# Optimization experiments

Hardware: AMD Instinct MI355X
Metric: run time of the kernel (lower is better)

## Reference

```python
import jax, jax.numpy as jnp
import numpy as np

B, N, F, H, E = 64, 64, 2, 1024, 65536
T_IN, T_OUT = 10, 6  # SAMPLING_INPUT_FRAMES, SAMPLING_OUTPUT_FRAMES
NT = B * N
THRESH, EXIST = 10.0, 0.04
MLP_DIMS = [(2048, H), (4096, 2048), (2048, 4096), (1024, 2048), (512, 1024), (F * N, 512)]


def setup_inputs():
    key = jax.random.key(0)
    ks = jax.random.split(key, 32)
    inp = {
        'feature_input': jax.random.normal(ks[0], (T_IN, NT, F), jnp.float32),
        'edge_indices_input': jax.random.randint(ks[1], (T_IN, 2, E), 0, NT),
        'edge_indices_output': jax.random.randint(ks[2], (T_OUT, 2, E), 0, NT),
        'number_of_trajectories': B,
        'stats': jax.random.uniform(ks[3], (2, F), jnp.float32, 0.5, 1.5),  # (std, mean)
        'w_gcn': jax.random.normal(ks[4], (F, F), jnp.float32) / np.sqrt(F),
        'b_gcn': jnp.zeros((F,), jnp.float32),
        'w_ih': jax.random.normal(ks[5], (4 * H, F * N), jnp.float32) / np.sqrt(F * N),
        'w_hh': jax.random.normal(ks[6], (4 * H, H), jnp.float32) / np.sqrt(H),
        'b_ih': jnp.zeros((4 * H,), jnp.float32),
        'b_hh': jnp.zeros((4 * H,), jnp.float32),
    }
    for i, (o, d) in enumerate(MLP_DIMS):
        inp[f'w{i+1}'] = jax.random.normal(ks[7 + i], (o, d), jnp.float32) / np.sqrt(d)
        inp[f'b{i+1}'] = jnp.zeros((o,), jnp.float32)
    return inp


def _gcn_edges(x, ei, W, b):
    # PyG GCNConv: out = D^{-1/2} (A + I) D^{-1/2} (x W^T) + b, edge list form
    xw = x @ W.T
    src, dst = ei[0], ei[1]
    n = x.shape[0]
    deg = 1.0 + jax.ops.segment_sum(jnp.ones_like(src, jnp.float32), dst, num_segments=n)
    dinv = jax.lax.rsqrt(deg)
    out = jax.ops.segment_sum(xw[src] * (dinv[src] * dinv[dst])[:, None], dst, num_segments=n)
    return out + xw * (dinv * dinv)[:, None] + b


def _gcn_dense(x, A, W, b):
    # x [B,N,F]; A [B,N,N] already contains self loops (find_edge_index output)
    deg = A.sum(-1)
    dinv = jnp.where(deg > 0, jax.lax.rsqrt(deg), 0.0)
    An = A * dinv[:, :, None] * dinv[:, None, :]
    return jnp.einsum('bij,bjf->bif', An, x @ W.T) + b


def _build_adj(pred, stats, bsz):
    # faithful to find_edge_index: denormalize, cdist<=10, existence mask, self-loops kept
    f = (pred * stats[0] + stats[1]).reshape(bsz, N, F)
    d2 = jnp.sum((f[:, :, None, :] - f[:, None, :, :]) ** 2, -1)
    mask = (jnp.sqrt(jnp.maximum(d2, 0.0)) <= THRESH).astype(jnp.float32)
    exist = ((f[..., 0] > EXIST) & (f[..., 1] > EXIST)).astype(jnp.float32)
    A = mask * exist[:, :, None] * exist[:, None, :]
    # gcn_norm's add_remaining_self_loops -> every node ends with a self loop
    return jnp.maximum(A, jnp.eye(N, dtype=A.dtype))


def _forward(feature_input, edge_indices_input, bsz, stats, w_gcn, b_gcn, w_ih, w_hh, b_ih, b_hh, mlp_params):
    h = jnp.zeros((bsz, H), feature_input.dtype)
    c = jnp.zeros((bsz, H), feature_input.dtype)

    def lstm(x, h, c):  # torch LSTM gate order i, f, g, o
        g = x @ w_ih.T + b_ih + h @ w_hh.T + b_hh
        i, f, gg, o = jnp.split(g, 4, axis=-1)
        c = jax.nn.sigmoid(f) * c + jax.nn.sigmoid(i) * jnp.tanh(gg)
        h = jax.nn.sigmoid(o) * jnp.tanh(c)
        return h, c

    def mlp(x):
        for w, b_ in mlp_params[:-1]:
            x = jax.nn.relu(x @ w.T + b_)
        w, b_ = mlp_params[-1]
        return x @ w.T + b_

    x_enc = [feature_input[0]]
    for i in range(T_IN - 1):  # torch loop breaks before last frame
        g = _gcn_edges(feature_input[i], edge_indices_input[i], w_gcn, b_gcn)
        h, c = lstm(g.reshape(bsz, F * N), h, c)
        x_enc.append(mlp(h).reshape(bsz * N, F))

    cur_x = feature_input[T_IN - 1]
    cur_ei = edge_indices_input[T_IN - 1]
    A = None
    y_dec = []
    for i in range(T_OUT):
        if i == 0:
            g = _gcn_edges(cur_x, cur_ei, w_gcn, b_gcn)
        else:
            g = _gcn_dense(cur_x.reshape(bsz, N, F), A, w_gcn, b_gcn).reshape(bsz * N, F)
        h, c = lstm(g.reshape(bsz, F * N), h, c)
        pred = mlp(h).reshape(bsz * N, F)
        y_dec.append(pred)
        cur_x = pred
        A = _build_adj(pred, stats, bsz)
    # [T_IN + T_OUT, B*N, F]: x_pred_encode stacked then y_pred_decode stacked
    return jnp.concatenate([jnp.stack(x_enc), jnp.stack(y_dec)], 0)


def reference(feature_input, edge_indices_input, edge_indices_output, number_of_trajectories, stats, w_gcn, b_gcn, w_ih, w_hh, b_ih, b_hh, w1, b1, w2, b2, w3, b3, w4, b4, w5, b5, w6, b6):
    mlp_params = [(w1, b1), (w2, b2), (w3, b3), (w4, b4), (w5, b5), (w6, b6)]
    return _forward(feature_input, edge_indices_input, number_of_trajectories, stats, w_gcn, b_gcn, w_ih, w_hh, b_ih, b_hh, mlp_params)
```

## Files before the change

kernel.cpp:

```cpp
#include <hip/hip_runtime.h>
#include <hip/hip_bf16.h>
#include <math.h>

#define NTOT 4096
#define NEDGE 65536
#define BSZ 64
#define NN 64
#define HDIM 1024
#define TIN 10
#define TOUT 6
#define FRAME_ELEMS (NTOT * 2)

typedef short s16x8 __attribute__((ext_vector_type(8)));
typedef float f32x4 __attribute__((ext_vector_type(4)));

__device__ __forceinline__ unsigned short f2bf(float f) {
    union { float f; unsigned u; } x; x.f = f;
    unsigned r = x.u + 0x7fffu + ((x.u >> 16) & 1u);
    return (unsigned short)(r >> 16);
}

struct TT { const float* W; float* WT; int NO; int K; int toff; };
struct TT8 { TT t[8]; };

__global__ __launch_bounds__(256) void transpose_all(TT8 tasks) {
    int bid = blockIdx.x;
    int ti = 0;
    #pragma unroll
    for (int j = 1; j < 8; ++j) if (bid >= tasks.t[j].toff) ti = j;
    TT tk = tasks.t[ti];
    int local = bid - tk.toff;
    int tilesK = tk.K >> 5;
    int kb = local % tilesK, nb = local / tilesK;
    int k0 = kb * 32, n0 = nb * 32;
    __shared__ float t[32][33];
    int tx = threadIdx.x & 31, ty = threadIdx.x >> 5;
    #pragma unroll
    for (int i = 0; i < 4; ++i)
        t[ty + i * 8][tx] = tk.W[(size_t)(n0 + ty + i * 8) * tk.K + k0 + tx];
    __syncthreads();
    #pragma unroll
    for (int i = 0; i < 4; ++i)
        tk.WT[(size_t)(k0 + ty + i * 8) * tk.NO + n0 + tx] = t[tx][ty + i * 8];
}


__global__ void bgcn_init_xw(const float* __restrict__ feat, const float* __restrict__ wg,
                             float* __restrict__ deg, float* __restrict__ xw) {
    int i = blockIdx.x * blockDim.x + threadIdx.x;
    if (i >= 10 * NTOT) return;
    deg[i] = 1.0f;
    float x0 = feat[i * 2], x1 = feat[i * 2 + 1];
    xw[i * 2]     = x0 * wg[0] + x1 * wg[1];
    xw[i * 2 + 1] = x0 * wg[2] + x1 * wg[3];
}

__global__ void bgcn_count(const int* __restrict__ ei, float* __restrict__ deg) {
    int e = blockIdx.x * blockDim.x + threadIdx.x;
    if (e >= 10 * NEDGE) return;
    int t = e >> 16, el = e & 65535;
    int dst = ei[t * 2 * NEDGE + NEDGE + el];
    atomicAdd(&deg[t * NTOT + dst], 1.0f);
}

__global__ void bgcn_node(const float* __restrict__ bg, float* __restrict__ deg,
                          const float* __restrict__ xw, float* __restrict__ gT_all) {
    int i = blockIdx.x * blockDim.x + threadIdx.x;
    if (i >= 10 * NTOT) return;
    float dinv = rsqrtf(deg[i]);
    deg[i] = dinv;
    int t = i >> 12, node = i & 4095;
    int b = node >> 6, nn = node & 63;
    float w2 = dinv * dinv;
    gT_all[t * 8192 + (nn * 2 + 0) * 64 + b] = xw[i * 2]     * w2 + bg[0];
    gT_all[t * 8192 + (nn * 2 + 1) * 64 + b] = xw[i * 2 + 1] * w2 + bg[1];
}

__global__ __launch_bounds__(256) void bgcn_scatter_lds(const int* __restrict__ ei,
                                                        const float* __restrict__ dinv,
                                                        const float* __restrict__ xw,
                                                        float* __restrict__ gT_all) {
    __shared__ float sg[8192];
    int t = blockIdx.x >> 3;
    int chunk = blockIdx.x & 7;
    for (int i = threadIdx.x; i < 8192; i += 256) sg[i] = 0.f;
    __syncthreads();
    const int* eis = ei + t * 2 * NEDGE;
    int e0 = chunk * 8192;
    for (int e = e0 + threadIdx.x; e < e0 + 8192; e += 256) {
        int s = eis[e];
        int d = eis[NEDGE + e];
        float w = dinv[t * NTOT + s] * dinv[t * NTOT + d];
        int b = d >> 6, nn = d & 63;
        atomicAdd(&sg[(nn * 2 + 0) * 64 + b], xw[(t * NTOT + s) * 2]     * w);
        atomicAdd(&sg[(nn * 2 + 1) * 64 + b], xw[(t * NTOT + s) * 2 + 1] * w);
    }
    __syncthreads();
    float* gt = gT_all + t * 8192;
    for (int i = threadIdx.x; i < 8192; i += 256) {
        float v = sg[i];
        if (v != 0.f) atomicAdd(&gt[i], v);
    }
}

template<int KC>
__global__ __launch_bounds__(256) void gemm_bx7(
    const float* __restrict__ inT, const float* __restrict__ inT2,
    const float* __restrict__ WT,  const float* __restrict__ WT2,
    float* __restrict__ P, int NO, int SK1)
{
    constexpr int STG = (KC > 64) ? 64 : KC;
    __shared__ float xs[STG * 64];
    int tid = threadIdx.x;
    int ks = blockIdx.y;
    const float* xsrc; const float* wsrc;
    if (ks < SK1) { xsrc = inT  + (size_t)ks * KC * 64;         wsrc = WT  + (size_t)ks * KC * NO; }
    else          { xsrc = inT2 + (size_t)(ks - SK1) * KC * 64; wsrc = WT2 + (size_t)(ks - SK1) * KC * NO; }
    int ns = tid >> 3, q = tid & 7;
    int n = blockIdx.x * 32 + ns;
    const float* xq = xs + q * 8;
    float acc[8];
    #pragma unroll
    for (int j = 0; j < 8; ++j) acc[j] = 0.f;

    for (int kb = 0; kb < KC; kb += STG) {
        if (kb) __syncthreads();
        #pragma unroll
        for (int i = 0; i < STG / 16; ++i)
            ((float4*)xs)[tid + i * 256] = ((const float4*)(xsrc + (size_t)kb * 64))[tid + i * 256];
        __syncthreads();
        const float* wp = wsrc + (size_t)kb * NO + n;
        float wbuf[4];
        #pragma unroll
        for (int kk = 0; kk < 4; ++kk) wbuf[kk] = wp[(size_t)kk * NO];
        for (int k = 0; k < STG; k += 4) {
            float wn[4] = {0.f, 0.f, 0.f, 0.f};
            if (k + 4 < STG) {
                #pragma unroll
                for (int kk = 0; kk < 4; ++kk) wn[kk] = wp[(size_t)(k + 4 + kk) * NO];
            }
            #pragma unroll
            for (int kk = 0; kk < 4; ++kk) {
                const float* xrow = xq + (k + kk) * 64;
                float w = wbuf[kk];
                float4 x0 = *(const float4*)(xrow + 0);
                float4 x1 = *(const float4*)(xrow + 4);
                acc[0] = fmaf(w, x0.x, acc[0]);  acc[1] = fmaf(w, x0.y, acc[1]);
                acc[2] = fmaf(w, x0.z, acc[2]);  acc[3] = fmaf(w, x0.w, acc[3]);
                acc[4] = fmaf(w, x1.x, acc[4]);  acc[5] = fmaf(w, x1.y, acc[5]);
                acc[6] = fmaf(w, x1.z, acc[6]);  acc[7] = fmaf(w, x1.w, acc[7]);
            }
            #pragma unroll
            for (int kk = 0; kk < 4; ++kk) wbuf[kk] = wn[kk];
        }
    }
    float* pp = P + ((size_t)ks * NO + n) * 64 + q * 8;
    *(float4*)(pp + 0) = make_float4(acc[0], acc[1], acc[2], acc[3]);
    *(float4*)(pp + 4) = make_float4(acc[4], acc[5], acc[6], acc[7]);
}

__global__ void reduce_relu_kernel(const float* __restrict__ P,
                                   const float* __restrict__ bias,
                                   float* __restrict__ aT,
                                   int NO, int SK, int relu) {
    int idx = blockIdx.x * blockDim.x + threadIdx.x;
    if (idx >= NO * 64) return;
    int n = idx >> 6;
    float v = bias[n];
    for (int ks = 0; ks < SK; ++ks) v += P[(size_t)ks * NO * 64 + idx];
    if (relu) v = fmaxf(v, 0.f);
    aT[idx] = v;
}

__global__ void lstm_update2(const float* __restrict__ P,
                             const float* __restrict__ b_ih, const float* __restrict__ b_hh,
                             float* __restrict__ hT, float* __restrict__ cT,
                             unsigned short* __restrict__ stash, int mbase) {
    int t = blockIdx.x * blockDim.x + threadIdx.x;
    if (t >= HDIM * BSZ) return;
    int j = t >> 6, b = t & 63;
    float g4[4];
    #pragma unroll
    for (int gi = 0; gi < 4; ++gi) {
        int row = gi * HDIM + j;
        float v = b_ih[row] + b_hh[row];
        size_t base = (size_t)row * 64 + b;
        #pragma unroll
        for (int ks = 0; ks < 9; ++ks) v += P[(size_t)ks * 4096 * 64 + base];
        g4[gi] = v;
    }
    float si = 1.f / (1.f + expf(-g4[0]));
    float sf = 1.f / (1.f + expf(-g4[1]));
    float gg = tanhf(g4[2]);
    float so = 1.f / (1.f + expf(-g4[3]));
    float cn = sf * cT[t] + si * gg;
    cT[t] = cn;
    float h = so * tanhf(cn);
    hT[t] = h;
    if (stash) stash[(size_t)(mbase + b) * HDIM + j] = f2bf(h);
}

__global__ void finalize3(const float* __restrict__ P, const float* __restrict__ b5,
                          const float* __restrict__ wt5, const float* __restrict__ b6,
                          const float* __restrict__ stats, const float* __restrict__ wg,
                          const float* __restrict__ bg,
                          float* __restrict__ frame, float* __restrict__ gT, int dec)
{
    int b = blockIdx.x;
    int n = threadIdx.x;
    __shared__ float a5[512];
    __shared__ float p[128];
    __shared__ float f0[NN], f1[NN], sxw0[NN], sxw1[NN], sdinv[NN];
    __shared__ int ex[NN];
    #pragma unroll
    for (int j = 0; j < 4; ++j) {
        int k = n * 4 + j;
        float v = b5[k];
        #pragma unroll 4
        for (int ks = 0; ks < 16; ++ks) v += P[((size_t)ks * 512 + k) * 64 + b];
        a5[k] = fmaxf(v, 0.f);
    }
    __syncthreads();
    float acc = b6[n];
    for (int k = 0; k < 512; ++k) acc = fmaf(a5[k], wt5[k * 128 + n], acc);
    p[n] = acc;
    frame[b * 128 + n] = acc;
    if (!dec) return;
    __syncthreads();
    int i = n;
    if (i < NN) {
        float p0 = p[i * 2], p1 = p[i * 2 + 1];
        float d0 = p0 * stats[0] + stats[2];
        float d1 = p1 * stats[1] + stats[3];
        f0[i] = d0; f1[i] = d1;
        ex[i] = (d0 > 0.04f) && (d1 > 0.04f);
        sxw0[i] = p0 * wg[0] + p1 * wg[1];
        sxw1[i] = p0 * wg[2] + p1 * wg[3];
    }
    __syncthreads();
    if (i < NN) {
        float fi0 = f0[i], fi1 = f1[i];
        int exi = ex[i];
        float deg = 0.f;
        for (int j = 0; j < NN; ++j) {
            float dx = fi0 - f0[j], dy = fi1 - f1[j];
            float a = (i == j) ? 1.0f :
                      ((dx * dx + dy * dy <= 100.0f && exi && ex[j]) ? 1.0f : 0.0f);
            deg += a;
        }
        sdinv[i] = rsqrtf(deg);
    }
    __syncthreads();
    if (i < NN) {
        float fi0 = f0[i], fi1 = f1[i];
        int exi = ex[i];
        float a0 = 0.f, a1 = 0.f;
        for (int j = 0; j < NN; ++j) {
            float dx = fi0 - f0[j], dy = fi1 - f1[j];
            float a = (i == j) ? 1.0f :
                      ((dx * dx + dy * dy <= 100.0f && exi && ex[j]) ? 1.0f : 0.0f);
            float an = a * sdinv[j];
            a0 += an * sxw0[j];
            a1 += an * sxw1[j];
        }
        float di = sdinv[i];
        gT[(i * 2 + 0) * 64 + b] = a0 * di + bg[0];
        gT[(i * 2 + 1) * 64 + b] = a1 * di + bg[1];
    }
}

struct PTasks {
    const float* W[6]; unsigned short* Bp[6]; int K[6]; int goff[7];
};
__global__ void pack_all(PTasks pt) {
    int g = blockIdx.x * blockDim.x + threadIdx.x;
    if (g >= pt.goff[6]) return;
    int l = 0;
    #pragma unroll
    for (int j = 1; j < 6; ++j) if (g >= pt.goff[j]) l = j;
    int local = g - pt.goff[l];
    int kgs = pt.K[l] >> 3;
    int kg = local % kgs;
    int n  = local / kgs;
    const float* src = pt.W[l] + (size_t)n * pt.K[l] + (size_t)kg * 8;
    unsigned short* dst = pt.Bp[l] + ((size_t)kg * (pt.goff[l + 1] - pt.goff[l]) / kgs + n) * 8;
    #pragma unroll
    for (int j = 0; j < 8; ++j) dst[j] = f2bf(src[j]);
}

__global__ __launch_bounds__(256) void gemm_mfma2(
    const unsigned short* __restrict__ inb,
    const unsigned short* __restrict__ Bp,
    const float* __restrict__ bias,
    unsigned short* __restrict__ outb,
    float* __restrict__ frames,
    float* __restrict__ accbuf,
    int K, int KC, int NO, int relu)
{
    __shared__ unsigned short A[64][72];
    int tid = threadIdx.x;
    int lane = tid & 63;
    int w = tid >> 6;
    int m0 = blockIdx.y * 64;
    int nb = blockIdx.x * 64;
    int koff = blockIdx.z * KC;
    int l15 = lane & 15;
    int lq  = lane >> 4;
    int n = nb + w * 16 + l15;
    int sm = tid >> 3, skq = tid & 7;
    const unsigned short* bpb = Bp + (size_t)(koff >> 3) * NO * 8;
    f32x4 acc[4] = {};

    {
        s16x8 a0 = *(const s16x8*)&inb[(size_t)(m0 + sm) * K + koff + skq * 8];
        s16x8 a1 = *(const s16x8*)&inb[(size_t)(m0 + sm + 32) * K + koff + skq * 8];
        *(s16x8*)&A[sm][skq * 8] = a0;
        *(s16x8*)&A[sm + 32][skq * 8] = a1;
    }
    __syncthreads();
    s16x8 b0 = *(const s16x8*)&bpb[((size_t)(0 + lq) * NO + n) * 8];
    s16x8 b1 = *(const s16x8*)&bpb[((size_t)(4 + lq) * NO + n) * 8];

    int nk = KC >> 6;
    for (int t = 0; t < nk; ++t) {
        s16x8 na0, na1, nb0, nb1;
        bool more = (t + 1 < nk);
        if (more) {
            int ko = koff + (t + 1) * 64;
            na0 = *(const s16x8*)&inb[(size_t)(m0 + sm) * K + ko + skq * 8];
            na1 = *(const s16x8*)&inb[(size_t)(m0 + sm + 32) * K + ko + skq * 8];
            int kg = (t + 1) * 8;
            nb0 = *(const s16x8*)&bpb[((size_t)(kg + lq) * NO + n) * 8];
            nb1 = *(const s16x8*)&bpb[((size_t)(kg + 4 + lq) * NO + n) * 8];
        }
        #pragma unroll
        for (int s = 0; s < 4; ++s) {
            s16x8 af = *(const s16x8*)&A[s * 16 + l15][lq * 8];
            acc[s] = __builtin_amdgcn_mfma_f32_16x16x32_bf16(af, b0, acc[s], 0, 0, 0);
        }
        #pragma unroll
        for (int s = 0; s < 4; ++s) {
            s16x8 af = *(const s16x8*)&A[s * 16 + l15][32 + lq * 8];
            acc[s] = __builtin_amdgcn_mfma_f32_16x16x32_bf16(af, b1, acc[s], 0, 0, 0);
        }
        if (more) {
            __syncthreads();
            *(s16x8*)&A[sm][skq * 8] = na0;
            *(s16x8*)&A[sm + 32][skq * 8] = na1;
            __syncthreads();
            b0 = nb0; b1 = nb1;
        }
    }
    if (accbuf) {
        #pragma unroll
        for (int s = 0; s < 4; ++s) {
            #pragma unroll
            for (int r = 0; r < 4; ++r) {
                int m = m0 + s * 16 + lq * 4 + r;
                atomicAdd(&accbuf[(size_t)m * NO + n], acc[s][r]);
            }
        }
        return;
    }
    float bn = bias[n];
    #pragma unroll
    for (int s = 0; s < 4; ++s) {
        #pragma unroll
        for (int r = 0; r < 4; ++r) {
            int m = m0 + s * 16 + lq * 4 + r;
            float v = acc[s][r] + bn;
            if (relu) v = fmaxf(v, 0.f);
            if (outb) outb[(size_t)m * NO + n] = f2bf(v);
            if (frames && m < 576) {
                int f = m >> 6, b = m & 63;
                frames[(size_t)f * FRAME_ELEMS + b * 128 + n] = v;
            }
        }
    }
}

__global__ void packrelu_kernel(const float* __restrict__ acc, const float* __restrict__ bias,
                                unsigned short* __restrict__ outb, int NO) {
    int idx = blockIdx.x * blockDim.x + threadIdx.x;
    if (idx >= 576 * NO) return;
    int n = idx & (NO - 1);
    float v = acc[idx] + bias[n];
    outb[idx] = f2bf(fmaxf(v, 0.f));
}


extern "C" void kernel_launch(void* const* d_in, const int* in_sizes, int n_in,
                              void* d_out, int out_size, void* d_ws, size_t ws_size,
                              hipStream_t stream) {
    const float* feat   = (const float*)d_in[0];
    const int*   ei_in  = (const int*)d_in[1];
    const float* stats  = (const float*)d_in[4];
    const float* w_gcn  = (const float*)d_in[5];
    const float* b_gcn  = (const float*)d_in[6];
    const float* w_ih   = (const float*)d_in[7];
    const float* w_hh   = (const float*)d_in[8];
    const float* b_ih   = (const float*)d_in[9];
    const float* b_hh   = (const float*)d_in[10];
    const float* wm[6], *bm[6];
    for (int i = 0; i < 6; ++i) { wm[i] = (const float*)d_in[11 + 2*i]; bm[i] = (const float*)d_in[12 + 2*i]; }
    const int mlp_K[6]  = {1024, 2048, 4096, 2048, 1024, 512};
    const int mlp_NO[6] = {2048, 4096, 2048, 1024, 512, 128};

    float* out = (float*)d_out;
    float* ws  = (float*)d_ws;

    size_t off = 0;
    float* wt_ih = ws + off; off += (size_t)128 * 4096;
    float* wt_hh = ws + off; off += (size_t)1024 * 4096;
    float* wt[6];
    const size_t wt_sz[6] = {(size_t)1024*2048, (size_t)2048*4096, (size_t)4096*2048,
                             (size_t)2048*1024, (size_t)1024*512, (size_t)512*128};
    for (int i = 0; i < 6; ++i) { wt[i] = ws + off; off += wt_sz[i]; }
    float* P      = ws + off; off += (size_t)32 * 2048 * 64;
    float* gT_all = ws + off; off += (size_t)10 * 128 * 64;
    float* gT_dec = ws + off; off += 8192;
    float* hT     = ws + off; off += 65536;
    float* cT     = ws + off; off += 65536;
    float* aT1    = ws + off; off += 131072;
    float* aT2    = ws + off; off += 262144;
    float* aT3    = aT1;
    float* aT4    = aT2;
    float* inb1f  = ws + off; off += 147456;
    float* deg    = inb1f;
    float* xw     = inb1f + 40960;
    size_t need_bytes = off * sizeof(float);
    if (ws_size < need_bytes) return;

    unsigned short* inb1 = (unsigned short*)inb1f;
    unsigned short* inb2 = (unsigned short*)P;
    unsigned short* inb3 = inb2 + (size_t)576 * 2048;
    unsigned short* inb4 = inb3 + (size_t)576 * 4096;
    unsigned short* inb5 = inb4 + (size_t)576 * 2048;
    unsigned short* inb6 = inb5 + (size_t)576 * 1024;
    unsigned short* Bp[6];
    {
        unsigned short* base = (unsigned short*)wt[0];
        size_t boff = 0;
        for (int l = 0; l < 6; ++l) { Bp[l] = base + boff; boff += (size_t)mlp_NO[l] * mlp_K[l]; }
    }
    float* accbuf = wt_hh;

    hipMemsetAsync(hT, 0, 2 * 65536 * sizeof(float), stream);
    hipMemcpyAsync(out, feat, FRAME_ELEMS * sizeof(float), hipMemcpyDeviceToDevice, stream);

    {
        TT8 tasks;
        const float* Wp[8] = {w_ih, w_hh, wm[0], wm[1], wm[2], wm[3], wm[4], wm[5]};
        float* WTp[8] = {wt_ih, wt_hh, wt[0], wt[1], wt[2], wt[3], wt[4], wt[5]};
        int NOs[8] = {4096, 4096, 2048, 4096, 2048, 1024, 512, 128};
        int Ks[8]  = {128, 1024, 1024, 2048, 4096, 2048, 1024, 512};
        int toff = 0;
        for (int j = 0; j < 8; ++j) {
            tasks.t[j] = {Wp[j], WTp[j], NOs[j], Ks[j], toff};
            toff += (Ks[j] >> 5) * (NOs[j] >> 5);
        }
        transpose_all<<<toff, 256, 0, stream>>>(tasks);
    }

    bgcn_init_xw<<<10 * NTOT / 256, 256, 0, stream>>>(feat, w_gcn, deg, xw);
    bgcn_count<<<10 * NEDGE / 256, 256, 0, stream>>>(ei_in, deg);
    bgcn_node<<<10 * NTOT / 256, 256, 0, stream>>>(b_gcn, deg, xw, gT_all);
    bgcn_scatter_lds<<<80, 256, 0, stream>>>(ei_in, deg, xw, gT_all);

    for (int s = 0; s < 15; ++s) {
        const float* gT_s = (s <= 9) ? (gT_all + (size_t)s * 8192) : gT_dec;

        gemm_bx7<128><<<dim3(128, 9), 256, 0, stream>>>(hT, gT_s, wt_hh, wt_ih, P, 4096, 8);
        lstm_update2<<<HDIM * BSZ / 256, 256, 0, stream>>>(
            P, b_ih, b_hh, hT, cT, (s <= 8) ? inb1 : nullptr, s * 64);

        if (s >= 9) {
            float* frame = out + (size_t)(s + 1) * FRAME_ELEMS;
            gemm_bx7<64><<<dim3(64, 16), 256, 0, stream>>>(hT, nullptr, wt[0], nullptr, P, 2048, 16);
            reduce_relu_kernel<<<2048 * 64 / 256, 256, 0, stream>>>(P, bm[0], aT1, 2048, 16, 1);
            gemm_bx7<256><<<dim3(128, 8), 256, 0, stream>>>(aT1, nullptr, wt[1], nullptr, P, 4096, 8);
            reduce_relu_kernel<<<4096 * 64 / 256, 256, 0, stream>>>(P, bm[1], aT2, 4096, 8, 1);
            gemm_bx7<256><<<dim3(64, 16), 256, 0, stream>>>(aT2, nullptr, wt[2], nullptr, P, 2048, 16);
            reduce_relu_kernel<<<2048 * 64 / 256, 256, 0, stream>>>(P, bm[2], aT3, 2048, 16, 1);
            gemm_bx7<128><<<dim3(32, 16), 256, 0, stream>>>(aT3, nullptr, wt[3], nullptr, P, 1024, 16);
            reduce_relu_kernel<<<1024 * 64 / 256, 256, 0, stream>>>(P, bm[3], aT4, 1024, 16, 1);
            gemm_bx7<64><<<dim3(16, 16), 256, 0, stream>>>(aT4, nullptr, wt[4], nullptr, P, 512, 16);
            finalize3<<<BSZ, 128, 0, stream>>>(P, bm[4], wt[5], bm[5], stats, w_gcn, b_gcn,
                                               frame, gT_dec, (s < 14) ? 1 : 0);
        }
    }

    {
        PTasks pt;
        int goff = 0;
        for (int l = 0; l < 6; ++l) {
            pt.W[l] = wm[l]; pt.Bp[l] = Bp[l]; pt.K[l] = mlp_K[l];
            pt.goff[l] = goff;
            goff += mlp_NO[l] * (mlp_K[l] >> 3);
        }
        pt.goff[6] = goff;
        pack_all<<<(goff + 255) / 256, 256, 0, stream>>>(pt);
    }
    unsigned short* chain_in[6]  = {inb1, inb2, inb3, inb4, inb5, inb6};
    unsigned short* chain_out[6] = {inb2, inb3, inb4, inb5, inb6, nullptr};
    const int mlp_SK[6] = {2, 4, 8, 4, 2, 1};
    for (int l = 0; l < 6; ++l) {
        int NO = mlp_NO[l], K = mlp_K[l], SK = mlp_SK[l], KC = K / SK;
        if (l < 5) {
            hipMemsetAsync(accbuf, 0, (size_t)576 * NO * sizeof(float), stream);
            gemm_mfma2<<<dim3(NO / 64, 9, SK), 256, 0, stream>>>(
                chain_in[l], Bp[l], bm[l], nullptr, nullptr, accbuf, K, KC, NO, 0);
            packrelu_kernel<<<(576 * NO + 255) / 256, 256, 0, stream>>>(
                accbuf, bm[l], chain_out[l], NO);
        } else {
            gemm_mfma2<<<dim3(NO / 64, 9, 1), 256, 0, stream>>>(
                chain_in[l], Bp[l], bm[l], nullptr, out + FRAME_ELEMS, nullptr, K, KC, NO, 0);
        }
    }
}
```

Baseline: 1.595 ms.

## Read weights in native row-major layout and drop most upfront transposes

The batched GEMM now reads weights directly in their original [NO, K] layout with per-row strides, loading float4 runs along K, instead of reading a pre-transposed copy. The transpose_all launch is reduced to only the small final MLP weight that finalize3 still needs. This removes the large one-time transpose pass over all LSTM and MLP weights. The cost is that lanes in a wavefront now read from different rows with a large stride, so weight loads are less coalesced than the previous contiguous-across-n pattern.

Result: faster. 1.326 ms (-16.9%).

```diff
diff --git a/kernel.cpp b/kernel.cpp
--- a/kernel.cpp
+++ b/kernel.cpp
@@ -104,20 +104,22 @@
 }
 
 template<int KC>
-__global__ __launch_bounds__(256) void gemm_bx7(
+__global__ __launch_bounds__(256) void gemm_bx8(
     const float* __restrict__ inT, const float* __restrict__ inT2,
-    const float* __restrict__ WT,  const float* __restrict__ WT2,
+    const float* __restrict__ W1,  const float* __restrict__ W2,
+    int st1, int st2,
     float* __restrict__ P, int NO, int SK1)
 {
     constexpr int STG = (KC > 64) ? 64 : KC;
     __shared__ float xs[STG * 64];
     int tid = threadIdx.x;
     int ks = blockIdx.y;
-    const float* xsrc; const float* wsrc;
-    if (ks < SK1) { xsrc = inT  + (size_t)ks * KC * 64;         wsrc = WT  + (size_t)ks * KC * NO; }
-    else          { xsrc = inT2 + (size_t)(ks - SK1) * KC * 64; wsrc = WT2 + (size_t)(ks - SK1) * KC * NO; }
+    const float* xsrc; const float* wrow; int koff, strideW;
+    if (ks < SK1) { xsrc = inT  + (size_t)ks * KC * 64;         wrow = W1; koff = ks * KC;         strideW = st1; }
+    else          { xsrc = inT2 + (size_t)(ks - SK1) * KC * 64; wrow = W2; koff = (ks - SK1) * KC; strideW = st2; }
     int ns = tid >> 3, q = tid & 7;
     int n = blockIdx.x * 32 + ns;
+    const float* wp0 = wrow + (size_t)n * strideW + koff;
     const float* xq = xs + q * 8;
     float acc[8];
     #pragma unroll
@@ -129,20 +131,17 @@
         for (int i = 0; i < STG / 16; ++i)
             ((float4*)xs)[tid + i * 256] = ((const float4*)(xsrc + (size_t)kb * 64))[tid + i * 256];
         __syncthreads();
-        const float* wp = wsrc + (size_t)kb * NO + n;
-        float wbuf[4];
-        #pragma unroll
-        for (int kk = 0; kk < 4; ++kk) wbuf[kk] = wp[(size_t)kk * NO];
-        for (int k = 0; k < STG; k += 4) {
-            float wn[4] = {0.f, 0.f, 0.f, 0.f};
-            if (k + 4 < STG) {
-                #pragma unroll
-                for (int kk = 0; kk < 4; ++kk) wn[kk] = wp[(size_t)(k + 4 + kk) * NO];
-            }
+        const float* wp = wp0 + kb;
+        float4 wA = *(const float4*)(wp + 0);
+        float4 wB = *(const float4*)(wp + 4);
+        for (int k = 0; k < STG; k += 8) {
+            float4 wC, wD;
+            if (k + 8 < STG)  wC = *(const float4*)(wp + k + 8);
+            if (k + 12 < STG) wD = *(const float4*)(wp + k + 12);
             #pragma unroll
             for (int kk = 0; kk < 4; ++kk) {
                 const float* xrow = xq + (k + kk) * 64;
-                float w = wbuf[kk];
+                float w = (kk == 0) ? wA.x : (kk == 1) ? wA.y : (kk == 2) ? wA.z : wA.w;
                 float4 x0 = *(const float4*)(xrow + 0);
                 float4 x1 = *(const float4*)(xrow + 4);
                 acc[0] = fmaf(w, x0.x, acc[0]);  acc[1] = fmaf(w, x0.y, acc[1]);
@@ -151,7 +150,17 @@
                 acc[6] = fmaf(w, x1.z, acc[6]);  acc[7] = fmaf(w, x1.w, acc[7]);
             }
             #pragma unroll
-            for (int kk = 0; kk < 4; ++kk) wbuf[kk] = wn[kk];
+            for (int kk = 0; kk < 4; ++kk) {
+                const float* xrow = xq + (k + 4 + kk) * 64;
+                float w = (kk == 0) ? wB.x : (kk == 1) ? wB.y : (kk == 2) ? wB.z : wB.w;
+                float4 x0 = *(const float4*)(xrow + 0);
+                float4 x1 = *(const float4*)(xrow + 4);
+                acc[0] = fmaf(w, x0.x, acc[0]);  acc[1] = fmaf(w, x0.y, acc[1]);
+                acc[2] = fmaf(w, x0.z, acc[2]);  acc[3] = fmaf(w, x0.w, acc[3]);
+                acc[4] = fmaf(w, x1.x, acc[4]);  acc[5] = fmaf(w, x1.y, acc[5]);
+                acc[6] = fmaf(w, x1.z, acc[6]);  acc[7] = fmaf(w, x1.w, acc[7]);
+            }
+            wA = wC; wB = wD;
         }
     }
     float* pp = P + ((size_t)ks * NO + n) * 64 + q * 8;
@@ -450,16 +459,9 @@
 
     {
         TT8 tasks;
-        const float* Wp[8] = {w_ih, w_hh, wm[0], wm[1], wm[2], wm[3], wm[4], wm[5]};
-        float* WTp[8] = {wt_ih, wt_hh, wt[0], wt[1], wt[2], wt[3], wt[4], wt[5]};
-        int NOs[8] = {4096, 4096, 2048, 4096, 2048, 1024, 512, 128};
-        int Ks[8]  = {128, 1024, 1024, 2048, 4096, 2048, 1024, 512};
-        int toff = 0;
-        for (int j = 0; j < 8; ++j) {
-            tasks.t[j] = {Wp[j], WTp[j], NOs[j], Ks[j], toff};
-            toff += (Ks[j] >> 5) * (NOs[j] >> 5);
-        }
-        transpose_all<<<toff, 256, 0, stream>>>(tasks);
+        tasks.t[0] = {wm[5], wt[5], 128, 512, 0};
+        for (int j = 1; j < 8; ++j) tasks.t[j] = {wm[5], wt[5], 128, 512, 64};
+        transpose_all<<<64, 256, 0, stream>>>(tasks);
     }
 
     bgcn_init_xw<<<10 * NTOT / 256, 256, 0, stream>>>(feat, w_gcn, deg, xw);
@@ -470,21 +472,21 @@
     for (int s = 0; s < 15; ++s) {
         const float* gT_s = (s <= 9) ? (gT_all + (size_t)s * 8192) : gT_dec;
 
-        gemm_bx7<128><<<dim3(128, 9), 256, 0, stream>>>(hT, gT_s, wt_hh, wt_ih, P, 4096, 8);
+        gemm_bx8<128><<<dim3(128, 9), 256, 0, stream>>>(hT, gT_s, w_hh, w_ih, 1024, 128, P, 4096, 8);
         lstm_update2<<<HDIM * BSZ / 256, 256, 0, stream>>>(
             P, b_ih, b_hh, hT, cT, (s <= 8) ? inb1 : nullptr, s * 64);
 
         if (s >= 9) {
             float* frame = out + (size_t)(s + 1) * FRAME_ELEMS;
-            gemm_bx7<64><<<dim3(64, 16), 256, 0, stream>>>(hT, nullptr, wt[0], nullptr, P, 2048, 16);
+            gemm_bx8<64><<<dim3(64, 16), 256, 0, stream>>>(hT, nullptr, wm[0], nullptr, 1024, 0, P, 2048, 16);
             reduce_relu_kernel<<<2048 * 64 / 256, 256, 0, stream>>>(P, bm[0], aT1, 2048, 16, 1);
-            gemm_bx7<256><<<dim3(128, 8), 256, 0, stream>>>(aT1, nullptr, wt[1], nullptr, P, 4096, 8);
+            gemm_bx8<256><<<dim3(128, 8), 256, 0, stream>>>(aT1, nullptr, wm[1], nullptr, 2048, 0, P, 4096, 8);
             reduce_relu_kernel<<<4096 * 64 / 256, 256, 0, stream>>>(P, bm[1], aT2, 4096, 8, 1);
-            gemm_bx7<256><<<dim3(64, 16), 256, 0, stream>>>(aT2, nullptr, wt[2], nullptr, P, 2048, 16);
+            gemm_bx8<256><<<dim3(64, 16), 256, 0, stream>>>(aT2, nullptr, wm[2], nullptr, 4096, 0, P, 2048, 16);
             reduce_relu_kernel<<<2048 * 64 / 256, 256, 0, stream>>>(P, bm[2], aT3, 2048, 16, 1);
-            gemm_bx7<128><<<dim3(32, 16), 256, 0, stream>>>(aT3, nullptr, wt[3], nullptr, P, 1024, 16);
+            gemm_bx8<128><<<dim3(32, 16), 256, 0, stream>>>(aT3, nullptr, wm[3], nullptr, 2048, 0, P, 1024, 16);
             reduce_relu_kernel<<<1024 * 64 / 256, 256, 0, stream>>>(P, bm[3], aT4, 1024, 16, 1);
-            gemm_bx7<64><<<dim3(16, 16), 256, 0, stream>>>(aT4, nullptr, wt[4], nullptr, P, 512, 16);
+            gemm_bx8<64><<<dim3(16, 16), 256, 0, stream>>>(aT4, nullptr, wm[4], nullptr, 1024, 0, P, 512, 16);
             finalize3<<<BSZ, 128, 0, stream>>>(P, bm[4], wt[5], bm[5], stats, w_gcn, b_gcn,
                                                frame, gT_dec, (s < 14) ? 1 : 0);
         }
```
